# Kernel tuning notes

Measured on AMD Instinct MI355X. Metric: run time of the kernel, lower is better.

The kernel has to match this reference:

```python
import jax, jax.numpy as jnp
import numpy as np

HEADS = 16
DIM_HEAD = 64
INNER = HEADS * DIM_HEAD  # 1024
QUERY_DIM = 1024
CONTEXT_DIM = 1024
TEXT_LEN = 77
IMG_SCALE = 1.0
SCALE = DIM_HEAD ** -0.5


def setup_inputs() -> dict:
    key = jax.random.key(0)
    ks = jax.random.split(key, 10)
    B, N, Lc = 16, 2048, 333  # 77 text + 256 image tokens
    x = jax.random.normal(ks[0], (B, N, QUERY_DIM), dtype=jnp.float32)
    context = jax.random.normal(ks[1], (B, Lc, CONTEXT_DIM), dtype=jnp.float32)
    def w(k, din, dout):
        return jax.random.normal(k, (din, dout), dtype=jnp.float32) * (din ** -0.5)
    Wq = w(ks[2], QUERY_DIM, INNER)
    Wk = w(ks[3], CONTEXT_DIM, INNER)
    Wv = w(ks[4], CONTEXT_DIM, INNER)
    Wk_ip = w(ks[5], CONTEXT_DIM, INNER)
    Wv_ip = w(ks[6], CONTEXT_DIM, INNER)
    Wo = w(ks[7], INNER, QUERY_DIM)
    bo = jnp.zeros((QUERY_DIM,), dtype=jnp.float32)
    return {"x": x, "context": context, "Wq": Wq, "Wk": Wk, "Wv": Wv,
            "Wk_ip": Wk_ip, "Wv_ip": Wv_ip, "Wo": Wo, "bo": bo}


def _attend(q, k, v):
    # q: [B,N,H,D], k/v: [B,L,H,D]
    sim = jnp.einsum('bihd,bjhd->bhij', q, k) * SCALE
    attn = jax.nn.softmax(sim, axis=-1)
    out = jnp.einsum('bhij,bjhd->bihd', attn, v)
    B, N, H, D = out.shape
    return out.reshape(B, N, H * D)


def reference(x, context, Wq, Wk, Wv, Wk_ip, Wv_ip, Wo, bo):
    B, N, _ = x.shape
    ctx_txt = context[:, :TEXT_LEN, :]
    ctx_img = context[:, TEXT_LEN:, :]
    q = (x @ Wq).reshape(B, N, HEADS, DIM_HEAD)
    k = (ctx_txt @ Wk).reshape(B, TEXT_LEN, HEADS, DIM_HEAD)
    v = (ctx_txt @ Wv).reshape(B, TEXT_LEN, HEADS, DIM_HEAD)
    out = _attend(q, k, v)
    Li = ctx_img.shape[1]
    k_ip = (ctx_img @ Wk_ip).reshape(B, Li, HEADS, DIM_HEAD)
    v_ip = (ctx_img @ Wv_ip).reshape(B, Li, HEADS, DIM_HEAD)
    out_ip = _attend(q, k_ip, v_ip)
    out = out + IMG_SCALE * out_ip
    return out @ Wo + bo
```

## Files before the change

### kernel.cpp

```cpp
#include <hip/hip_runtime.h>
#include <cstdint>
#include <type_traits>

typedef unsigned short u16;
typedef __attribute__((ext_vector_type(8))) short short8;
typedef __attribute__((ext_vector_type(4))) float f32x4;

__device__ __forceinline__ u16 f2bf(float f) {
  unsigned x;
  __builtin_memcpy(&x, &f, 4);
  x = x + 0x7fffu + ((x >> 16) & 1u);
  return (u16)(x >> 16);
}
__device__ __forceinline__ f32x4 mfma16(short8 a, short8 b, f32x4 c) {
  return __builtin_amdgcn_mfma_f32_16x16x32_bf16(a, b, c, 0, 0, 0);
}
__device__ __forceinline__ void async_cp16(const u16* g, const u16* l) {
  __builtin_amdgcn_global_load_lds(
      (const __attribute__((address_space(1))) unsigned int*)(uintptr_t)g,
      (__attribute__((address_space(3))) unsigned int*)(uintptr_t)l, 16, 0, 0);
}

__global__ __launch_bounds__(256)
void cvt_f32_bf16(const float* __restrict__ s, u16* __restrict__ d, long n4) {
  long i = (long)blockIdx.x * 256 + threadIdx.x;
  if (i < n4) {
    float4 f = ((const float4*)s)[i];
    ushort4 o;
    o.x = f2bf(f.x);
    o.y = f2bf(f.y);
    o.z = f2bf(f.z);
    o.w = f2bf(f.w);
    ((ushort4*)d)[i] = o;
  }
}

struct TP { const float* s[6]; u16* d[6]; };

__global__ __launch_bounds__(256)
void transpose6(TP a) {
  __shared__ float tile[32][33];
  const float* S = a.s[blockIdx.z];
  u16* D = a.d[blockIdx.z];
  const int tx = threadIdx.x, ty = threadIdx.y;
  const int bx = blockIdx.x * 32, by = blockIdx.y * 32;
#pragma unroll
  for (int i = 0; i < 32; i += 8)
    tile[ty + i][tx] = S[(long)(by + ty + i) * 1024 + bx + tx];
  __syncthreads();
#pragma unroll
  for (int i = 0; i < 32; i += 8)
    D[(long)(bx + ty + i) * 1024 + by + tx] = f2bf(tile[tx][ty + i]);
}

template <typename CT>
__global__ __launch_bounds__(256, 2)
void gemm_bt(const u16* __restrict__ A, const u16* __restrict__ Bt0,
             const u16* __restrict__ Bt1, CT* __restrict__ C0,
             CT* __restrict__ C1, const float* __restrict__ bias,
             int M, int RPB, int BSTR, int ROFF) {
  const u16* Bt = (blockIdx.z == 0) ? Bt0 : Bt1;
  CT* C = (blockIdx.z == 0) ? C0 : C1;
  __shared__ u16 As[128 * 32];
  __shared__ u16 Bs[128 * 32];
  const int t = threadIdx.x;
  const int w = t >> 6, lane = t & 63;
  const int m0 = blockIdx.x * 128, n0 = blockIdx.y * 128;
  const int subk = (lane & 3) * 8;

  long ag[2], bg[2];
  int lo[2];
#pragma unroll
  for (int r = 0; r < 2; ++r) {
    int m = m0 + r * 64 + w * 16 + (lane >> 2);
    if (m >= M) m = M - 1;
    long row = (long)(m / RPB) * BSTR + (m % RPB) + ROFF;
    ag[r] = row * 1024 + subk;
    lo[r] = r * 2048 + w * 512 + (lane >> 2) * 32 + subk;
    int n = n0 + r * 64 + w * 16 + (lane >> 2);
    bg[r] = (long)n * 1024 + subk;
  }
  const int wm = w >> 1, wn = w & 1;
  const int lr = lane & 15, quad = lane >> 4;
  const u16* Ap = As + (wm * 64 + lr) * 32 + quad * 8;
  const u16* Bp = Bs + (wn * 64 + lr) * 32 + quad * 8;

  const f32x4 fz = {0.f, 0.f, 0.f, 0.f};
  f32x4 acc[4][4];
#pragma unroll
  for (int i = 0; i < 4; ++i)
#pragma unroll
    for (int j = 0; j < 4; ++j) acc[i][j] = fz;

  for (int k0 = 0; k0 < 1024; k0 += 32) {
    __syncthreads();
    async_cp16(A + ag[0] + k0, As + lo[0]);
    async_cp16(A + ag[1] + k0, As + lo[1]);
    async_cp16(Bt + bg[0] + k0, Bs + lo[0]);
    async_cp16(Bt + bg[1] + k0, Bs + lo[1]);
    __syncthreads();
    short8 a[4], b[4];
#pragma unroll
    for (int i = 0; i < 4; ++i) a[i] = *(const short8*)(Ap + i * 512);
#pragma unroll
    for (int i = 0; i < 4; ++i) b[i] = *(const short8*)(Bp + i * 512);
#pragma unroll
    for (int i = 0; i < 4; ++i)
#pragma unroll
      for (int j = 0; j < 4; ++j) acc[i][j] = mfma16(a[i], b[j], acc[i][j]);
  }

#pragma unroll
  for (int i = 0; i < 4; ++i) {
#pragma unroll
    for (int r = 0; r < 4; ++r) {
      int m = m0 + wm * 64 + i * 16 + quad * 4 + r;
      if (m < M) {
        long crow = ((long)(m / RPB) * BSTR + (m % RPB) + ROFF) * 1024;
#pragma unroll
        for (int j = 0; j < 4; ++j) {
          int n = n0 + wn * 64 + j * 16 + lr;
          float v = acc[i][j][r];
          if (bias) v += bias[n];
          if constexpr (std::is_same<CT, float>::value)
            C[crow + n] = v;
          else
            C[crow + n] = f2bf(v);
        }
      }
    }
  }
}

template <int L, int LP, int KOFF>
__device__ __forceinline__ void attn_phase(const u16* __restrict__ kbh,
                                           const u16* __restrict__ vbh,
                                           u16* Vt, u16* Pb, const short8* aq,
                                           f32x4* oacc, int t, int w, int lr,
                                           int quad) {
  constexpr int JT = LP / 16;
  __syncthreads();
  for (int idx = t; idx < LP * 8; idx += 256) {
    int j = idx >> 3, dg = idx & 7;
    short8 v = {0, 0, 0, 0, 0, 0, 0, 0};
    if (j < L) v = *(const short8*)(vbh + (long)(KOFF + j) * 1024 + dg * 8);
#pragma unroll
    for (int e = 0; e < 8; ++e) Vt[(dg * 8 + e) * 264 + j] = (u16)v[e];
  }
  __syncthreads();

  f32x4 sacc[JT];
#pragma unroll
  for (int jt = 0; jt < JT; ++jt) {
    const u16* kp = kbh + (long)(KOFF + jt * 16 + lr) * 1024;
    short8 b0 = *(const short8*)(kp + quad * 8);
    short8 b1 = *(const short8*)(kp + 32 + quad * 8);
    f32x4 z = {0.f, 0.f, 0.f, 0.f};
    z = mfma16(aq[0], b0, z);
    sacc[jt] = mfma16(aq[1], b1, z);
  }
#pragma unroll
  for (int r = 0; r < 4; ++r) {
    float mx = -3.0e38f;
#pragma unroll
    for (int jt = 0; jt < JT; ++jt) {
      int j = jt * 16 + lr;
      float v = (j < L) ? sacc[jt][r] * 0.125f : -3.0e38f;
      sacc[jt][r] = v;
      mx = fmaxf(mx, v);
    }
#pragma unroll
    for (int d = 1; d < 16; d <<= 1) mx = fmaxf(mx, __shfl_xor(mx, d, 64));
    float s = 0.f;
#pragma unroll
    for (int jt = 0; jt < JT; ++jt) {
      float p = __expf(sacc[jt][r] - mx);
      sacc[jt][r] = p;
      s += p;
    }
#pragma unroll
    for (int d = 1; d < 16; d <<= 1) s += __shfl_xor(s, d, 64);
    float is = 1.0f / s;
    int row = w * 16 + quad * 4 + r;
#pragma unroll
    for (int jt = 0; jt < JT; ++jt)
      Pb[row * 264 + jt * 16 + lr] = f2bf(sacc[jt][r] * is);
  }
#pragma unroll
  for (int c = 0; c < JT / 2; ++c) {
    short8 pf = *(const short8*)(Pb + (w * 16 + lr) * 264 + c * 32 + quad * 8);
#pragma unroll
    for (int nt = 0; nt < 4; ++nt) {
      short8 vf = *(const short8*)(Vt + (nt * 16 + lr) * 264 + c * 32 + quad * 8);
      oacc[nt] = mfma16(pf, vf, oacc[nt]);
    }
  }
}

__global__ __launch_bounds__(256, 2)
void attn_kernel(u16* __restrict__ q, const u16* __restrict__ kall,
                 const u16* __restrict__ vall) {
  __shared__ u16 Vt[64 * 264];
  __shared__ u16 Pb[64 * 264];
  const int t = threadIdx.x;
  const int w = t >> 6, lane = t & 63;
  const int lr = lane & 15, quad = lane >> 4;
  const int bq = blockIdx.x, h = blockIdx.y, b = blockIdx.z;
  const long qrow = (long)(b * 2048 + bq * 64 + w * 16 + lr) * 1024 + h * 64;
  short8 aq[2];
  aq[0] = *(const short8*)(q + qrow + quad * 8);
  aq[1] = *(const short8*)(q + qrow + 32 + quad * 8);
  const f32x4 fz = {0.f, 0.f, 0.f, 0.f};
  f32x4 oacc[4];
#pragma unroll
  for (int i = 0; i < 4; ++i) oacc[i] = fz;
  const u16* kbh = kall + (long)b * 333 * 1024 + h * 64;
  const u16* vbh = vall + (long)b * 333 * 1024 + h * 64;
  attn_phase<77, 96, 0>(kbh, vbh, Vt, Pb, aq, oacc, t, w, lr, quad);
  attn_phase<256, 256, 77>(kbh, vbh, Vt, Pb, aq, oacc, t, w, lr, quad);
#pragma unroll
  for (int nt = 0; nt < 4; ++nt)
#pragma unroll
    for (int r = 0; r < 4; ++r) {
      long row = (long)(b * 2048 + bq * 64 + w * 16 + quad * 4 + r);
      q[row * 1024 + h * 64 + nt * 16 + lr] = f2bf(oacc[nt][r]);
    }
}

extern "C" void kernel_launch(void* const* d_in, const int* in_sizes, int n_in,
                              void* d_out, int out_size, void* d_ws,
                              size_t ws_size, hipStream_t stream) {
  const float* x = (const float*)d_in[0];
  const float* ctx = (const float*)d_in[1];
  u16* ws = (u16*)d_ws;
  u16* WT[6];
  for (int i = 0; i < 6; ++i) WT[i] = ws + (size_t)i * (1u << 20);
  u16* xb = ws + (size_t)6 * (1u << 20);
  u16* qb = xb + (size_t)(1u << 25);
  u16* ctxb = qb + (size_t)(1u << 25);
  u16* kall = ctxb + (size_t)16 * 333 * 1024;
  u16* vall = kall + (size_t)16 * 333 * 1024;
  float* out = (float*)d_out;

  cvt_f32_bf16<<<dim3(32768), dim3(256), 0, stream>>>(x, xb, 8388608);
  cvt_f32_bf16<<<dim3(5328), dim3(256), 0, stream>>>(ctx, ctxb, 1363968);

  TP tp;
  tp.s[0] = (const float*)d_in[2]; tp.d[0] = WT[0];
  tp.s[1] = (const float*)d_in[3]; tp.d[1] = WT[1];
  tp.s[2] = (const float*)d_in[4]; tp.d[2] = WT[2];
  tp.s[3] = (const float*)d_in[5]; tp.d[3] = WT[3];
  tp.s[4] = (const float*)d_in[6]; tp.d[4] = WT[4];
  tp.s[5] = (const float*)d_in[7]; tp.d[5] = WT[5];
  transpose6<<<dim3(32, 32, 6), dim3(32, 8, 1), 0, stream>>>(tp);

  gemm_bt<u16><<<dim3(256, 8, 1), dim3(256), 0, stream>>>(
      xb, WT[0], WT[0], qb, qb, (const float*)nullptr, 32768, 2048, 2048, 0);
  gemm_bt<u16><<<dim3(10, 8, 2), dim3(256), 0, stream>>>(
      ctxb, WT[1], WT[2], kall, vall, (const float*)nullptr, 1232, 77, 333, 0);
  gemm_bt<u16><<<dim3(32, 8, 2), dim3(256), 0, stream>>>(
      ctxb, WT[3], WT[4], kall, vall, (const float*)nullptr, 4096, 256, 333, 77);
  attn_kernel<<<dim3(32, 16, 16), dim3(256), 0, stream>>>(qb, kall, vall);
  gemm_bt<float><<<dim3(256, 8, 1), dim3(256), 0, stream>>>(
      qb, WT[5], WT[5], out, out, (const float*)d_in[8], 32768, 2048, 2048, 0);
}
```

Measured before the change: 764.1 us.

## Write V pre-transposed from projection GEMM and chunk image attention with online softmax

```diff
diff --git a/kernel.cpp b/kernel.cpp
--- a/kernel.cpp
+++ b/kernel.cpp
@@ -35,6 +35,15 @@
   }
 }
 
+__global__ __launch_bounds__(256)
+void zero16(u16* __restrict__ p, long n8) {
+  long i = (long)blockIdx.x * 256 + threadIdx.x;
+  if (i < n8) {
+    short8 z = {0, 0, 0, 0, 0, 0, 0, 0};
+    ((short8*)p)[i] = z;
+  }
+}
+
 struct TP { const float* s[6]; u16* d[6]; };
 
 __global__ __launch_bounds__(256)
@@ -53,12 +62,12 @@
     D[(long)(bx + ty + i) * 1024 + by + tx] = f2bf(tile[tx][ty + i]);
 }
 
-template <typename CT>
+template <typename CT, bool VT>
 __global__ __launch_bounds__(256, 2)
 void gemm_bt(const u16* __restrict__ A, const u16* __restrict__ Bt0,
              const u16* __restrict__ Bt1, CT* __restrict__ C0,
              CT* __restrict__ C1, const float* __restrict__ bias,
-             int M, int RPB, int BSTR, int ROFF) {
+             int M, int RPB, int BSTR, int ROFF, int vtcol) {
   const u16* Bt = (blockIdx.z == 0) ? Bt0 : Bt1;
   CT* C = (blockIdx.z == 0) ? C0 : C1;
   __shared__ u16 As[128 * 32];
@@ -110,6 +119,26 @@
       for (int j = 0; j < 4; ++j) acc[i][j] = mfma16(a[i], b[j], acc[i][j]);
   }
 
+  if constexpr (VT) {
+    if (blockIdx.z == 1) {
+#pragma unroll
+      for (int i = 0; i < 4; ++i)
+#pragma unroll
+        for (int r = 0; r < 4; ++r) {
+          int m = m0 + wm * 64 + i * 16 + quad * 4 + r;
+          if (m < M) {
+            long vrow = (long)(m / RPB) * 1024;
+            int j = m % RPB;
+#pragma unroll
+            for (int jj = 0; jj < 4; ++jj) {
+              int n = n0 + wn * 64 + jj * 16 + lr;
+              C[(vrow + n) * 384 + vtcol + j] = (CT)f2bf(acc[i][jj][r]);
+            }
+          }
+        }
+      return;
+    }
+  }
 #pragma unroll
   for (int i = 0; i < 4; ++i) {
 #pragma unroll
@@ -132,99 +161,157 @@
   }
 }
 
-template <int L, int LP, int KOFF>
-__device__ __forceinline__ void attn_phase(const u16* __restrict__ kbh,
-                                           const u16* __restrict__ vbh,
-                                           u16* Vt, u16* Pb, const short8* aq,
-                                           f32x4* oacc, int t, int w, int lr,
-                                           int quad) {
-  constexpr int JT = LP / 16;
+__device__ __forceinline__ void stage_vt(const u16* __restrict__ vrow,
+                                         int colbase, u16* Vt, int t) {
+#pragma unroll
+  for (int it = 0; it < 4; ++it) {
+    int G = it * 256 + t;
+    int r = G >> 4, p = G & 15;
+    int g = p ^ (r & 7);
+    async_cp16(vrow + (long)r * 384 + colbase + g * 8, Vt + G * 8);
+  }
+}
+
+template <int JT>
+__device__ __forceinline__ void qk_mm(const u16* __restrict__ kbase, short8 aq0,
+                                      short8 aq1, int lr, int quad,
+                                      f32x4* sacc) {
+#pragma unroll
+  for (int jt = 0; jt < JT; ++jt) {
+    const u16* kp = kbase + (long)(jt * 16 + lr) * 1024 + quad * 8;
+    short8 b0 = *(const short8*)kp;
+    short8 b1 = *(const short8*)(kp + 32);
+    f32x4 z = {0.f, 0.f, 0.f, 0.f};
+    z = mfma16(aq0, b0, z);
+    sacc[jt] = mfma16(aq1, b1, z);
+  }
+}
+
+template <int JT>
+__device__ __forceinline__ void pv_mm(const u16* Vt, const u16* Pb, int w,
+                                      int lr, int quad, f32x4* oacc) {
+#pragma unroll
+  for (int c = 0; c < JT / 2; ++c) {
+    short8 pf = *(const short8*)(Pb + (w * 16 + lr) * 136 + c * 32 + quad * 8);
+#pragma unroll
+    for (int nt = 0; nt < 4; ++nt) {
+      int g = (c * 4 + quad) ^ (lr & 7);
+      short8 vf = *(const short8*)(Vt + (nt * 16 + lr) * 128 + g * 8);
+      oacc[nt] = mfma16(pf, vf, oacc[nt]);
+    }
+  }
+}
+
+__device__ __forceinline__ void img_chunk(int koff, int colbase,
+                                          const u16* __restrict__ kbh,
+                                          const u16* __restrict__ vbh, u16* Vt,
+                                          u16* Pb, short8 aq0, short8 aq1,
+                                          f32x4 (&oi)[4], float (&mrun)[4],
+                                          float (&lrun)[4], int t, int w,
+                                          int lr, int quad) {
   __syncthreads();
-  for (int idx = t; idx < LP * 8; idx += 256) {
-    int j = idx >> 3, dg = idx & 7;
-    short8 v = {0, 0, 0, 0, 0, 0, 0, 0};
-    if (j < L) v = *(const short8*)(vbh + (long)(KOFF + j) * 1024 + dg * 8);
-#pragma unroll
-    for (int e = 0; e < 8; ++e) Vt[(dg * 8 + e) * 264 + j] = (u16)v[e];
-  }
-  __syncthreads();
-
-  f32x4 sacc[JT];
-#pragma unroll
-  for (int jt = 0; jt < JT; ++jt) {
-    const u16* kp = kbh + (long)(KOFF + jt * 16 + lr) * 1024;
-    short8 b0 = *(const short8*)(kp + quad * 8);
-    short8 b1 = *(const short8*)(kp + 32 + quad * 8);
-    f32x4 z = {0.f, 0.f, 0.f, 0.f};
-    z = mfma16(aq[0], b0, z);
-    sacc[jt] = mfma16(aq[1], b1, z);
-  }
+  stage_vt(vbh, colbase, Vt, t);
+  f32x4 sacc[8];
+  qk_mm<8>(kbh + (long)koff * 1024, aq0, aq1, lr, quad, sacc);
 #pragma unroll
   for (int r = 0; r < 4; ++r) {
-    float mx = -3.0e38f;
-#pragma unroll
-    for (int jt = 0; jt < JT; ++jt) {
-      int j = jt * 16 + lr;
-      float v = (j < L) ? sacc[jt][r] * 0.125f : -3.0e38f;
+    float mprev = mrun[r];
+    float mx = mprev;
+#pragma unroll
+    for (int jt = 0; jt < 8; ++jt) {
+      float v = sacc[jt][r] * 0.125f;
       sacc[jt][r] = v;
       mx = fmaxf(mx, v);
     }
 #pragma unroll
     for (int d = 1; d < 16; d <<= 1) mx = fmaxf(mx, __shfl_xor(mx, d, 64));
+    float sc = __expf(mprev - mx);
+    int row = w * 16 + quad * 4 + r;
     float s = 0.f;
 #pragma unroll
-    for (int jt = 0; jt < JT; ++jt) {
+    for (int jt = 0; jt < 8; ++jt) {
       float p = __expf(sacc[jt][r] - mx);
-      sacc[jt][r] = p;
       s += p;
+      Pb[row * 136 + jt * 16 + lr] = f2bf(p);
     }
 #pragma unroll
     for (int d = 1; d < 16; d <<= 1) s += __shfl_xor(s, d, 64);
-    float is = 1.0f / s;
-    int row = w * 16 + quad * 4 + r;
-#pragma unroll
-    for (int jt = 0; jt < JT; ++jt)
-      Pb[row * 264 + jt * 16 + lr] = f2bf(sacc[jt][r] * is);
-  }
-#pragma unroll
-  for (int c = 0; c < JT / 2; ++c) {
-    short8 pf = *(const short8*)(Pb + (w * 16 + lr) * 264 + c * 32 + quad * 8);
-#pragma unroll
-    for (int nt = 0; nt < 4; ++nt) {
-      short8 vf = *(const short8*)(Vt + (nt * 16 + lr) * 264 + c * 32 + quad * 8);
-      oacc[nt] = mfma16(pf, vf, oacc[nt]);
-    }
-  }
-}
-
-__global__ __launch_bounds__(256, 2)
+    lrun[r] = lrun[r] * sc + s;
+    mrun[r] = mx;
+#pragma unroll
+    for (int nt = 0; nt < 4; ++nt) oi[nt][r] *= sc;
+  }
+  __syncthreads();
+  pv_mm<8>(Vt, Pb, w, lr, quad, oi);
+}
+
+__global__ __launch_bounds__(256, 4)
 void attn_kernel(u16* __restrict__ q, const u16* __restrict__ kall,
-                 const u16* __restrict__ vall) {
-  __shared__ u16 Vt[64 * 264];
-  __shared__ u16 Pb[64 * 264];
+                 const u16* __restrict__ vtg) {
+  __shared__ u16 Vt[64 * 128];
+  __shared__ u16 Pb[64 * 136];
   const int t = threadIdx.x;
   const int w = t >> 6, lane = t & 63;
   const int lr = lane & 15, quad = lane >> 4;
   const int bq = blockIdx.x, h = blockIdx.y, b = blockIdx.z;
   const long qrow = (long)(b * 2048 + bq * 64 + w * 16 + lr) * 1024 + h * 64;
-  short8 aq[2];
-  aq[0] = *(const short8*)(q + qrow + quad * 8);
-  aq[1] = *(const short8*)(q + qrow + 32 + quad * 8);
+  short8 aq0 = *(const short8*)(q + qrow + quad * 8);
+  short8 aq1 = *(const short8*)(q + qrow + 32 + quad * 8);
   const f32x4 fz = {0.f, 0.f, 0.f, 0.f};
-  f32x4 oacc[4];
-#pragma unroll
-  for (int i = 0; i < 4; ++i) oacc[i] = fz;
+  f32x4 ot[4], oi[4];
+#pragma unroll
+  for (int i = 0; i < 4; ++i) { ot[i] = fz; oi[i] = fz; }
+  float mrun[4], lrun[4];
+#pragma unroll
+  for (int r = 0; r < 4; ++r) { mrun[r] = -3.0e38f; lrun[r] = 0.f; }
   const u16* kbh = kall + (long)b * 333 * 1024 + h * 64;
-  const u16* vbh = vall + (long)b * 333 * 1024 + h * 64;
-  attn_phase<77, 96, 0>(kbh, vbh, Vt, Pb, aq, oacc, t, w, lr, quad);
-  attn_phase<256, 256, 77>(kbh, vbh, Vt, Pb, aq, oacc, t, w, lr, quad);
-#pragma unroll
-  for (int nt = 0; nt < 4; ++nt)
+  const u16* vbh = vtg + (long)(b * 16 + h) * 64 * 384;
+
+  stage_vt(vbh, 0, Vt, t);
+  {
+    f32x4 sacc[6];
+    qk_mm<6>(kbh, aq0, aq1, lr, quad, sacc);
 #pragma unroll
     for (int r = 0; r < 4; ++r) {
-      long row = (long)(b * 2048 + bq * 64 + w * 16 + quad * 4 + r);
-      q[row * 1024 + h * 64 + nt * 16 + lr] = f2bf(oacc[nt][r]);
-    }
+      float mx = -3.0e38f;
+#pragma unroll
+      for (int jt = 0; jt < 6; ++jt) {
+        int j = jt * 16 + lr;
+        float v = (j < 77) ? sacc[jt][r] * 0.125f : -3.0e38f;
+        sacc[jt][r] = v;
+        mx = fmaxf(mx, v);
+      }
+#pragma unroll
+      for (int d = 1; d < 16; d <<= 1) mx = fmaxf(mx, __shfl_xor(mx, d, 64));
+      float s = 0.f;
+#pragma unroll
+      for (int jt = 0; jt < 6; ++jt) {
+        float p = __expf(sacc[jt][r] - mx);
+        sacc[jt][r] = p;
+        s += p;
+      }
+#pragma unroll
+      for (int d = 1; d < 16; d <<= 1) s += __shfl_xor(s, d, 64);
+      float is = 1.0f / s;
+      int row = w * 16 + quad * 4 + r;
+#pragma unroll
+      for (int jt = 0; jt < 6; ++jt)
+        Pb[row * 136 + jt * 16 + lr] = f2bf(sacc[jt][r] * is);
+    }
+    __syncthreads();
+    pv_mm<6>(Vt, Pb, w, lr, quad, ot);
+  }
+  img_chunk(77, 96, kbh, vbh, Vt, Pb, aq0, aq1, oi, mrun, lrun, t, w, lr, quad);
+  img_chunk(205, 224, kbh, vbh, Vt, Pb, aq0, aq1, oi, mrun, lrun, t, w, lr, quad);
+
+#pragma unroll
+  for (int r = 0; r < 4; ++r) {
+    float il = 1.0f / lrun[r];
+    long row = (long)(b * 2048 + bq * 64 + w * 16 + quad * 4 + r);
+#pragma unroll
+    for (int nt = 0; nt < 4; ++nt)
+      q[row * 1024 + h * 64 + nt * 16 + lr] = f2bf(ot[nt][r] + oi[nt][r] * il);
+  }
 }
 
 extern "C" void kernel_launch(void* const* d_in, const int* in_sizes, int n_in,
@@ -239,7 +326,7 @@
   u16* qb = xb + (size_t)(1u << 25);
   u16* ctxb = qb + (size_t)(1u << 25);
   u16* kall = ctxb + (size_t)16 * 333 * 1024;
-  u16* vall = kall + (size_t)16 * 333 * 1024;
+  u16* vtg = xb;
   float* out = (float*)d_out;
 
   cvt_f32_bf16<<<dim3(32768), dim3(256), 0, stream>>>(x, xb, 8388608);
@@ -254,13 +341,14 @@
   tp.s[5] = (const float*)d_in[7]; tp.d[5] = WT[5];
   transpose6<<<dim3(32, 32, 6), dim3(32, 8, 1), 0, stream>>>(tp);
 
-  gemm_bt<u16><<<dim3(256, 8, 1), dim3(256), 0, stream>>>(
-      xb, WT[0], WT[0], qb, qb, (const float*)nullptr, 32768, 2048, 2048, 0);
-  gemm_bt<u16><<<dim3(10, 8, 2), dim3(256), 0, stream>>>(
-      ctxb, WT[1], WT[2], kall, vall, (const float*)nullptr, 1232, 77, 333, 0);
-  gemm_bt<u16><<<dim3(32, 8, 2), dim3(256), 0, stream>>>(
-      ctxb, WT[3], WT[4], kall, vall, (const float*)nullptr, 4096, 256, 333, 77);
-  attn_kernel<<<dim3(32, 16, 16), dim3(256), 0, stream>>>(qb, kall, vall);
-  gemm_bt<float><<<dim3(256, 8, 1), dim3(256), 0, stream>>>(
-      qb, WT[5], WT[5], out, out, (const float*)d_in[8], 32768, 2048, 2048, 0);
-}
+  gemm_bt<u16, false><<<dim3(256, 8, 1), dim3(256), 0, stream>>>(
+      xb, WT[0], WT[0], qb, qb, (const float*)nullptr, 32768, 2048, 2048, 0, -1);
+  zero16<<<dim3(3072), dim3(256), 0, stream>>>(vtg, 786432);
+  gemm_bt<u16, true><<<dim3(10, 8, 2), dim3(256), 0, stream>>>(
+      ctxb, WT[1], WT[2], kall, vtg, (const float*)nullptr, 1232, 77, 333, 0, 0);
+  gemm_bt<u16, true><<<dim3(32, 8, 2), dim3(256), 0, stream>>>(
+      ctxb, WT[3], WT[4], kall, vtg, (const float*)nullptr, 4096, 256, 333, 77, 96);
+  attn_kernel<<<dim3(32, 16, 16), dim3(256), 0, stream>>>(qb, kall, vtg);
+  gemm_bt<float, false><<<dim3(256, 8, 1), dim3(256), 0, stream>>>(
+      qb, WT[5], WT[5], out, out, (const float*)d_in[8], 32768, 2048, 2048, 0, -1);
+}
```

Result: faster. 704.8 us (-7.8%).
